# Optimization experiments

Measured on AMD Instinct MI355X. Metric: run time of the kernel, lower is better.

Reference implementation:

```python
import jax, jax.numpy as jnp
import numpy as np

N_NODES = 20000
N_EDGES = 320000
N_GRAPHS = 64
OBS = 64
EDGE_DIM = 16
HEADS = 4
HID = 64
NEG_SLOPE = 0.2
EPS = 1e-16


def _gat_layer(x, src, dst, edge_attr, W, We, att_src, att_dst, att_edge, b):
    """PyG GATConv (concat=True, eval mode: no dropout).
    x: [N, Fin], edge_attr: [E, De], W: [Fin, H*C], We: [De, H*C],
    att_*: [H, C], b: [H*C]. Returns [N, H*C]."""
    N = x.shape[0]
    h = (x @ W).reshape(N, HEADS, HID)                      # [N,H,C]
    he = (edge_attr @ We).reshape(-1, HEADS, HID)           # [E,H,C]
    a_src = jnp.einsum('nhc,hc->nh', h, att_src)            # [N,H]
    a_dst = jnp.einsum('nhc,hc->nh', h, att_dst)
    a_e = jnp.einsum('ehc,hc->eh', he, att_edge)            # [E,H]
    alpha = a_src[src] + a_dst[dst] + a_e                   # [E,H]
    alpha = jax.nn.leaky_relu(alpha, NEG_SLOPE)
    # segment softmax over destination neighborhoods
    m = jax.ops.segment_max(alpha, dst, num_segments=N)     # [N,H]
    m = jnp.where(jnp.isfinite(m), m, 0.0)
    ea = jnp.exp(alpha - m[dst])
    denom = jax.ops.segment_sum(ea, dst, num_segments=N)    # [N,H]
    alpha = ea / (denom[dst] + EPS)
    msg = h[src] * alpha[:, :, None]                        # [E,H,C]
    out = jax.ops.segment_sum(msg, dst, num_segments=N)     # [N,H,C]
    return out.reshape(N, HEADS * HID) + b


def _make_params(key):
    ks = jax.random.split(key, 18)
    p = {}
    dims_in = [OBS, HEADS * HID, HEADS * HID]
    for i in range(3):
        j = i * 6
        fin = dims_in[i]
        p[f'W{i+1}'] = jax.random.normal(ks[j], (fin, HEADS * HID), jnp.float32) * (1.0 / np.sqrt(fin))
        p[f'We{i+1}'] = jax.random.normal(ks[j+1], (EDGE_DIM, HEADS * HID), jnp.float32) * (1.0 / np.sqrt(EDGE_DIM))
        p[f'att_src{i+1}'] = jax.random.normal(ks[j+2], (HEADS, HID), jnp.float32) * 0.1
        p[f'att_dst{i+1}'] = jax.random.normal(ks[j+3], (HEADS, HID), jnp.float32) * 0.1
        p[f'att_edge{i+1}'] = jax.random.normal(ks[j+4], (HEADS, HID), jnp.float32) * 0.1
        p[f'b{i+1}'] = jnp.zeros((HEADS * HID,), jnp.float32)
    return p


def setup_inputs() -> dict:
    key = jax.random.key(0)
    k1, k2, k3, k4, kp = jax.random.split(key, 5)
    inp = {
        'x': jax.random.normal(k1, (N_NODES, OBS), jnp.float32),
        'edge_index': jax.random.randint(k2, (2, N_EDGES), 0, N_NODES, jnp.int64),
        'edge_attr': jax.random.normal(k3, (N_EDGES, EDGE_DIM), jnp.float32),
        'batch': jnp.sort(jax.random.randint(k4, (N_NODES,), 0, N_GRAPHS, jnp.int64)),
    }
    inp.update(_make_params(kp))
    return inp


def reference(x, edge_index, edge_attr, batch,
              W1, We1, att_src1, att_dst1, att_edge1, b1,
              W2, We2, att_src2, att_dst2, att_edge2, b2,
              W3, We3, att_src3, att_dst3, att_edge3, b3):
    src, dst = edge_index[0], edge_index[1]
    h = jax.nn.relu(_gat_layer(x, src, dst, edge_attr, W1, We1, att_src1, att_dst1, att_edge1, b1))
    h = jax.nn.relu(_gat_layer(h, src, dst, edge_attr, W2, We2, att_src2, att_dst2, att_edge2, b2))
    h = jax.nn.relu(_gat_layer(h, src, dst, edge_attr, W3, We3, att_src3, att_dst3, att_edge3, b3))
    # global mean pool over graphs
    sums = jax.ops.segment_sum(h, batch, num_segments=N_GRAPHS)      # [G, H*C]
    counts = jax.ops.segment_sum(jnp.ones((h.shape[0], 1), h.dtype), batch, num_segments=N_GRAPHS)
    pooled = sums / jnp.maximum(counts, 1.0)
    return jnp.tanh(pooled)
```

## Files before the change

kernel.cpp:

```cpp
#include <hip/hip_runtime.h>
#include <hip/hip_bf16.h>
#include <hip/hip_fp16.h>
#include <math.h>

#define N_NODES 20000
#define N_EDGES 320000
#define N_GRAPHS 64
#define OBS 64
#define EDGE_DIM 16
#define HEADS 4
#define HID 64
#define HC 256
#define NEG_SLOPE 0.2f
#define EPSF 1e-16f
#define N_SCAN_BLOCKS ((N_NODES + 255) / 256)
#define CVT_BLOCKS (N_NODES * OBS / 4 / 256)
#define CAP 64

typedef _Float16 f16x8 __attribute__((ext_vector_type(8)));
typedef float f32x4 __attribute__((ext_vector_type(4)));

#define SB_ZERO  N_SCAN_BLOCKS
#define SB_CVT   (SB_ZERO + CVT_BLOCKS)
#define SB_WT0   (SB_CVT + OBS)
#define SB_WT1   (SB_WT0 + HC)
#define SB_WT2   (SB_WT1 + HC)
#define SB_TOT   (SB_WT2 + 3)
__global__ __launch_bounds__(256) void setup_kernel(int* __restrict__ counts,
                                                    float* __restrict__ pooled,
                                                    int* __restrict__ gcounts,
                                                    const float* __restrict__ x, __half* __restrict__ x16,
                                                    const float* __restrict__ W0, const float* __restrict__ W1,
                                                    const float* __restrict__ W2,
                                                    __half* __restrict__ wt0, __half* __restrict__ wt1,
                                                    __half* __restrict__ wt2,
                                                    const float* __restrict__ We0, const float* __restrict__ ae0,
                                                    const float* __restrict__ We1, const float* __restrict__ ae1,
                                                    const float* __restrict__ We2, const float* __restrict__ ae2,
                                                    float* __restrict__ w_eff3) {
    int b = blockIdx.x, t = threadIdx.x;
    if (b < SB_ZERO) {
        int i = b * 256 + t;
        if (i < N_NODES) counts[i] = 0;
        if (i < N_GRAPHS * HC) pooled[i] = 0.f;
        if (i < N_GRAPHS) gcounts[i] = 0;
    } else if (b < SB_CVT) {
        int i = ((b - SB_ZERO) * 256 + t) * 4;
        float4 v = *(const float4*)(x + i);
        *(__half2*)(x16 + i)     = __floats2half2_rn(v.x, v.y);
        *(__half2*)(x16 + i + 2) = __floats2half2_rn(v.z, v.w);
    } else if (b < SB_WT0) {
        int k = b - SB_CVT;
        wt0[(size_t)t * OBS + k] = __float2half(W0[(size_t)k * HC + t]);
    } else if (b < SB_WT1) {
        int k = b - SB_WT0;
        wt1[(size_t)t * HC + k] = __float2half(W1[(size_t)k * HC + t]);
    } else if (b < SB_WT2) {
        int k = b - SB_WT1;
        wt2[(size_t)t * HC + k] = __float2half(W2[(size_t)k * HC + t]);
    } else {
        int l = b - SB_WT2;
        if (t >= 64) return;
        const float* We = (l == 0) ? We0 : (l == 1) ? We1 : We2;
        const float* ae = (l == 0) ? ae0 : (l == 1) ? ae1 : ae2;
        int hh = t >> 4, d = t & 15;
        float acc = 0.f;
        #pragma unroll 8
        for (int c = 0; c < HID; ++c)
            acc += We[d * HC + hh * HID + c] * ae[hh * HID + c];
        w_eff3[l * 64 + hh * 16 + d] = acc;
    }
}

__global__ __launch_bounds__(256) void count_kernel(const int* __restrict__ ei, int* __restrict__ counts) {
    int e = blockIdx.x * 256 + threadIdx.x;
    if (e >= N_EDGES) return;
    atomicAdd(&counts[ei[N_EDGES + e]], 1);
}

__global__ __launch_bounds__(256) void scan_local_kernel(const int* __restrict__ counts,
                                                         int* __restrict__ row_start,
                                                         int* __restrict__ blk_tot) {
    int b = blockIdx.x, t = threadIdx.x;
    int i = b * 256 + t;
    int v = (i < N_NODES) ? counts[i] : 0;
    int lane = t & 63, w = t >> 6;
    int x = v;
    #pragma unroll
    for (int off = 1; off < 64; off <<= 1) {
        int y = __shfl_up(x, off, 64);
        if (lane >= off) x += y;
    }
    __shared__ int wsum[4];
    __shared__ int woff[4];
    if (lane == 63) wsum[w] = x;
    __syncthreads();
    if (t == 0) {
        int s = 0;
        #pragma unroll
        for (int k = 0; k < 4; ++k) { woff[k] = s; s += wsum[k]; }
        blk_tot[b] = s;
    }
    __syncthreads();
    if (i < N_NODES) row_start[i] = x - v + woff[w];
}

__global__ __launch_bounds__(256) void scan_add_kernel(int* __restrict__ row_start,
                                                       const int* __restrict__ blk_tot,
                                                       int* __restrict__ cursor) {
    __shared__ int sd[128];
    int b = blockIdx.x, t = threadIdx.x;
    if (t < 128) sd[t] = (t < b && t < N_SCAN_BLOCKS) ? blk_tot[t] : 0;
    __syncthreads();
    #pragma unroll
    for (int off = 64; off >= 1; off >>= 1) {
        if (t < off) sd[t] += sd[t + off];
        __syncthreads();
    }
    int base = sd[0];
    int i = b * 256 + t;
    if (i < N_NODES) {
        int r = row_start[i] + base;
        row_start[i] = r;
        cursor[i] = r;
    }
}

__global__ __launch_bounds__(256) void fill_ae_kernel(const int* __restrict__ ei,
                                                      const float* __restrict__ edge_attr,
                                                      const float* __restrict__ w_eff3,
                                                      int* __restrict__ cursor,
                                                      int* __restrict__ src_csr,
                                                      float4* __restrict__ ae_csr) {
    __shared__ float wsh[192];
    int t = threadIdx.x;
    if (t < 192) wsh[t] = w_eff3[t];
    __syncthreads();
    int e = blockIdx.x * 256 + t;
    if (e >= N_EDGES) return;
    int s = ei[e];
    int d = ei[N_EDGES + e];
    int pos = atomicAdd(&cursor[d], 1);
    src_csr[pos] = s;
    const float* ea = edge_attr + (size_t)e * EDGE_DIM;
    float x[16];
    #pragma unroll
    for (int i = 0; i < 16; i += 4) {
        float4 v = *(const float4*)(ea + i);
        x[i] = v.x; x[i + 1] = v.y; x[i + 2] = v.z; x[i + 3] = v.w;
    }
    #pragma unroll
    for (int l = 0; l < 3; ++l) {
        float al[4];
        #pragma unroll
        for (int hh = 0; hh < 4; ++hh) {
            float acc = 0.f;
            #pragma unroll
            for (int i = 0; i < 16; ++i) acc += x[i] * wsh[l * 64 + hh * 16 + i];
            al[hh] = acc;
        }
        ae_csr[(size_t)l * N_EDGES + pos] = make_float4(al[0], al[1], al[2], al[3]);
    }
}

template <int NKT>
__global__ __launch_bounds__(256) void gemm16_kernel(const __half* __restrict__ A16,
                                                     const __half* __restrict__ Wt16,
                                                     __half* __restrict__ C16, int M,
                                                     const float* __restrict__ att_src,
                                                     const float* __restrict__ att_dst,
                                                     float* __restrict__ a_src,
                                                     float* __restrict__ a_dst) {
    constexpr int K = NKT * 32;
    __shared__ __align__(16) _Float16 lds[64 * 264];
    int t = threadIdx.x;
    int w = t >> 6, l = t & 63;
    int cg = l & 15, gg = l >> 4;
    int m0 = blockIdx.x * 64;

    {
        int row = (t >> 6) * 16 + (t & 15);
        int k8 = (t >> 4) & 3;
        int rg = m0 + row;
        if (rg >= M) rg = M - 1;
        const _Float16* ag = (const _Float16*)A16 + (size_t)rg * K + k8 * 8;
        f16x8 tmp[NKT];
        #pragma unroll
        for (int j = 0; j < NKT; ++j) tmp[j] = *(const f16x8*)(ag + j * 32);
        #pragma unroll
        for (int j = 0; j < NKT; ++j) *(f16x8*)&lds[(size_t)(j * 256 + t) * 8] = tmp[j];
    }
    __syncthreads();

    f32x4 acc[4][4] = {};
    const _Float16* bg = (const _Float16*)Wt16 + (size_t)(w * 64 + cg) * K + gg * 8;
    #pragma unroll 2
    for (int kt = 0; kt < NKT; ++kt) {
        f16x8 bf[4], af[4];
        #pragma unroll
        for (int ni = 0; ni < 4; ++ni)
            bf[ni] = *(const f16x8*)(bg + (size_t)(ni * 16) * K + kt * 32);
        #pragma unroll
        for (int mi = 0; mi < 4; ++mi)
            af[mi] = *(const f16x8*)&lds[(size_t)(kt * 256 + mi * 64 + l) * 8];
        #pragma unroll
        for (int mi = 0; mi < 4; ++mi)
            #pragma unroll
            for (int ni = 0; ni < 4; ++ni)
                acc[mi][ni] = __builtin_amdgcn_mfma_f32_16x16x32_f16(af[mi], bf[ni], acc[mi][ni], 0, 0, 0);
    }

    {
        float avs[4], avd[4];
        #pragma unroll
        for (int ni = 0; ni < 4; ++ni) {
            avs[ni] = att_src[w * 64 + ni * 16 + cg];
            avd[ni] = att_dst[w * 64 + ni * 16 + cg];
        }
        #pragma unroll
        for (int mi = 0; mi < 4; ++mi)
            #pragma unroll
            for (int reg = 0; reg < 4; ++reg) {
                float ps = acc[mi][0][reg] * avs[0] + acc[mi][1][reg] * avs[1]
                         + acc[mi][2][reg] * avs[2] + acc[mi][3][reg] * avs[3];
                float pd = acc[mi][0][reg] * avd[0] + acc[mi][1][reg] * avd[1]
                         + acc[mi][2][reg] * avd[2] + acc[mi][3][reg] * avd[3];
                #pragma unroll
                for (int o = 1; o < 16; o <<= 1) {
                    ps += __shfl_xor(ps, o, 64);
                    pd += __shfl_xor(pd, o, 64);
                }
                int m = m0 + mi * 16 + gg * 4 + reg;
                if (cg == 0 && m < M) {
                    a_src[(size_t)m * 4 + w] = ps;
                    a_dst[(size_t)m * 4 + w] = pd;
                }
            }
    }

    __syncthreads();
    #pragma unroll
    for (int mi = 0; mi < 4; ++mi)
        #pragma unroll
        for (int ni = 0; ni < 4; ++ni)
            #pragma unroll
            for (int reg = 0; reg < 4; ++reg) {
                int row = mi * 16 + gg * 4 + reg;
                int col = w * 64 + ni * 16 + cg;
                lds[row * 264 + col] = (_Float16)acc[mi][ni][reg];
            }
    __syncthreads();
    #pragma unroll
    for (int i = 0; i < 8; ++i) {
        int g = i * 256 + t;
        int row = g >> 5, cw = g & 31;
        int m = m0 + row;
        if (m < M) {
            f16x8 v = *(const f16x8*)&lds[row * 264 + cw * 8];
            *(f16x8*)((_Float16*)C16 + (size_t)m * HC + cw * 8) = v;
        }
    }
}

__global__ __launch_bounds__(256) void aggregate4_kernel(const int* __restrict__ src_csr,
                                                         const float4* __restrict__ ae_csr,
                                                         const int* __restrict__ row_start,
                                                         const int* __restrict__ counts,
                                                         const float* __restrict__ a_src,
                                                         const float* __restrict__ a_dst,
                                                         const __half* __restrict__ h16,
                                                         const float* __restrict__ bias,
                                                         __half* __restrict__ out16) {
    __shared__ float wlds[4][4][CAP + 1];
    int wid = threadIdx.x >> 6, lane = threadIdx.x & 63;
    int n = blockIdx.x * 4 + wid;
    int start = row_start[n];
    int deg = counts[n];
    const float4* ae = ae_csr + start;
    const int* sp = src_csr + start;
    float4 ad = *(const float4*)(a_dst + (size_t)n * 4);

    float m0 = -INFINITY, m1 = -INFINITY, m2 = -INFINITY, m3 = -INFINITY;
    for (int i = lane; i < deg; i += 64) {
        float4 a = ae[i];
        int s = sp[i];
        float4 as = *(const float4*)(a_src + (size_t)s * 4);
        float v0 = a.x + as.x + ad.x; v0 = v0 > 0.f ? v0 : NEG_SLOPE * v0;
        float v1 = a.y + as.y + ad.y; v1 = v1 > 0.f ? v1 : NEG_SLOPE * v1;
        float v2 = a.z + as.z + ad.z; v2 = v2 > 0.f ? v2 : NEG_SLOPE * v2;
        float v3 = a.w + as.w + ad.w; v3 = v3 > 0.f ? v3 : NEG_SLOPE * v3;
        if (i < CAP) {
            wlds[wid][0][i] = v0; wlds[wid][1][i] = v1;
            wlds[wid][2][i] = v2; wlds[wid][3][i] = v3;
        }
        m0 = fmaxf(m0, v0); m1 = fmaxf(m1, v1);
        m2 = fmaxf(m2, v2); m3 = fmaxf(m3, v3);
    }
    #pragma unroll
    for (int o = 32; o > 0; o >>= 1) {
        m0 = fmaxf(m0, __shfl_xor(m0, o, 64));
        m1 = fmaxf(m1, __shfl_xor(m1, o, 64));
        m2 = fmaxf(m2, __shfl_xor(m2, o, 64));
        m3 = fmaxf(m3, __shfl_xor(m3, o, 64));
    }

    float d0 = 0.f, d1 = 0.f, d2 = 0.f, d3 = 0.f;
    for (int i = lane; i < deg; i += 64) {
        float v0, v1, v2, v3;
        if (i < CAP) {
            v0 = wlds[wid][0][i]; v1 = wlds[wid][1][i];
            v2 = wlds[wid][2][i]; v3 = wlds[wid][3][i];
        } else {
            float4 a = ae[i];
            int s = sp[i];
            float4 as = *(const float4*)(a_src + (size_t)s * 4);
            v0 = a.x + as.x + ad.x; v0 = v0 > 0.f ? v0 : NEG_SLOPE * v0;
            v1 = a.y + as.y + ad.y; v1 = v1 > 0.f ? v1 : NEG_SLOPE * v1;
            v2 = a.z + as.z + ad.z; v2 = v2 > 0.f ? v2 : NEG_SLOPE * v2;
            v3 = a.w + as.w + ad.w; v3 = v3 > 0.f ? v3 : NEG_SLOPE * v3;
        }
        float e0 = __expf(v0 - m0);
        float e1 = __expf(v1 - m1);
        float e2 = __expf(v2 - m2);
        float e3 = __expf(v3 - m3);
        d0 += e0; d1 += e1; d2 += e2; d3 += e3;
        if (i < CAP) {
            wlds[wid][0][i] = e0; wlds[wid][1][i] = e1;
            wlds[wid][2][i] = e2; wlds[wid][3][i] = e3;
        }
    }
    #pragma unroll
    for (int o = 32; o > 0; o >>= 1) {
        d0 += __shfl_xor(d0, o, 64);
        d1 += __shfl_xor(d1, o, 64);
        d2 += __shfl_xor(d2, o, 64);
        d3 += __shfl_xor(d3, o, 64);
    }

    int g = lane >> 5, j = lane & 31;
    int head = j >> 3;
    float mh = (head < 2) ? (head == 0 ? m0 : m1) : (head == 2 ? m2 : m3);
    float dh = (head < 2) ? (head == 0 ? d0 : d1) : (head == 2 ? d2 : d3);
    float adh = (head < 2) ? (head == 0 ? ad.x : ad.y) : (head == 2 ? ad.z : ad.w);

    float acc[8] = {};
    int niter = (deg + 1) >> 1;
    if (deg <= CAP) {
        int it = 0;
        for (; it + 4 <= niter; it += 4) {
            int s_[4]; float w_[4]; f16x8 hv_[4];
            #pragma unroll
            for (int u = 0; u < 4; ++u) {
                int e = (it + u) * 2 + g;
                bool valid = e < deg;
                int ec = valid ? e : deg - 1;
                s_[u] = sp[ec];
                float wv = wlds[wid][head][ec];
                w_[u] = valid ? wv : 0.f;
            }
            #pragma unroll
            for (int u = 0; u < 4; ++u)
                hv_[u] = *(const f16x8*)((const _Float16*)h16 + (size_t)s_[u] * HC + j * 8);
            #pragma unroll
            for (int u = 0; u < 4; ++u)
                #pragma unroll
                for (int q = 0; q < 8; ++q) acc[q] += w_[u] * (float)hv_[u][q];
        }
        for (; it < niter; ++it) {
            int e = it * 2 + g;
            bool valid = e < deg;
            int ec = valid ? e : deg - 1;
            int s = sp[ec];
            float wv = wlds[wid][head][ec];
            float wgt = valid ? wv : 0.f;
            f16x8 hv = *(const f16x8*)((const _Float16*)h16 + (size_t)s * HC + j * 8);
            #pragma unroll
            for (int q = 0; q < 8; ++q) acc[q] += wgt * (float)hv[q];
        }
    } else {
        for (int it = 0; it < niter; ++it) {
            int e = it * 2 + g;
            bool valid = e < deg;
            int ec = valid ? e : deg - 1;
            int s = sp[ec];
            float wgt;
            if (ec < CAP) {
                wgt = wlds[wid][head][ec];
            } else {
                float4 a = ae[ec];
                float aa = (head < 2) ? (head == 0 ? a.x : a.y) : (head == 2 ? a.z : a.w);
                const float* asp = a_src + (size_t)s * 4;
                float v = aa + asp[head] + adh;
                v = v > 0.f ? v : NEG_SLOPE * v;
                wgt = __expf(v - mh);
            }
            if (!valid) wgt = 0.f;
            f16x8 hv = *(const f16x8*)((const _Float16*)h16 + (size_t)s * HC + j * 8);
            #pragma unroll
            for (int q = 0; q < 8; ++q) acc[q] += wgt * (float)hv[q];
        }
    }
    #pragma unroll
    for (int q = 0; q < 8; ++q) acc[q] += __shfl_xor(acc[q], 32, 64);

    if (g == 0) {
        float invd = 1.f / (dh + EPSF);
        float4 b0 = *(const float4*)(bias + j * 8);
        float4 b1 = *(const float4*)(bias + j * 8 + 4);
        float r[8];
        r[0] = fmaxf(acc[0] * invd + b0.x, 0.f);
        r[1] = fmaxf(acc[1] * invd + b0.y, 0.f);
        r[2] = fmaxf(acc[2] * invd + b0.z, 0.f);
        r[3] = fmaxf(acc[3] * invd + b0.w, 0.f);
        r[4] = fmaxf(acc[4] * invd + b1.x, 0.f);
        r[5] = fmaxf(acc[5] * invd + b1.y, 0.f);
        r[6] = fmaxf(acc[6] * invd + b1.z, 0.f);
        r[7] = fmaxf(acc[7] * invd + b1.w, 0.f);
        f16x8 o;
        #pragma unroll
        for (int q = 0; q < 8; ++q) o[q] = (_Float16)r[q];
        *(f16x8*)((_Float16*)out16 + (size_t)n * HC + j * 8) = o;
    }
}

#define NPB 100
__global__ __launch_bounds__(256) void pool_kernel(const __half* __restrict__ h,
                                                   const int* __restrict__ batch,
                                                   float* __restrict__ pooled,
                                                   int* __restrict__ gcounts) {
    int t = threadIdx.x;
    int n0 = blockIdx.x * NPB;
    int n1 = n0 + NPB;
    if (n1 > N_NODES) n1 = N_NODES;
    if (n0 >= N_NODES) return;
    int cur = batch[n0];
    float acc = 0.f;
    int cnt = 0;
    for (int n = n0; n < n1; ++n) {
        int g = batch[n];
        if (g != cur) {
            atomicAdd(&pooled[cur * HC + t], acc);
            if (t == 0) atomicAdd(&gcounts[cur], cnt);
            acc = 0.f; cnt = 0; cur = g;
        }
        acc += __half2float(h[(size_t)n * HC + t]);
        cnt++;
    }
    atomicAdd(&pooled[cur * HC + t], acc);
    if (t == 0) atomicAdd(&gcounts[cur], cnt);
}

__global__ __launch_bounds__(256) void finalize_kernel(const float* __restrict__ pooled,
                                                       const int* __restrict__ gcounts,
                                                       float* __restrict__ out) {
    int g = blockIdx.x, t = threadIdx.x;
    float c = (float)(gcounts[g] > 1 ? gcounts[g] : 1);
    out[g * HC + t] = tanhf(pooled[g * HC + t] / c);
}

extern "C" void kernel_launch(void* const* d_in, const int* in_sizes, int n_in,
                              void* d_out, int out_size, void* d_ws, size_t ws_size,
                              hipStream_t stream) {
    const float* x         = (const float*)d_in[0];
    const int*   ei        = (const int*)d_in[1];
    const float* edge_attr = (const float*)d_in[2];
    const int*   batch     = (const int*)d_in[3];
    const float* Wl[3]  = {(const float*)d_in[4],  (const float*)d_in[10], (const float*)d_in[16]};
    const float* Wel[3] = {(const float*)d_in[5],  (const float*)d_in[11], (const float*)d_in[17]};
    const float* asl[3] = {(const float*)d_in[6],  (const float*)d_in[12], (const float*)d_in[18]};
    const float* adl[3] = {(const float*)d_in[7],  (const float*)d_in[13], (const float*)d_in[19]};
    const float* ael[3] = {(const float*)d_in[8],  (const float*)d_in[14], (const float*)d_in[20]};
    const float* bl[3]  = {(const float*)d_in[9],  (const float*)d_in[15], (const float*)d_in[21]};
    float* out = (float*)d_out;

    char* p = (char*)d_ws;
    auto alloc = [&](size_t bytes) -> void* {
        void* r = (void*)p;
        p += (bytes + 255) & ~(size_t)255;
        return r;
    };
    __half* x16       = (__half*)alloc((size_t)N_NODES * OBS * 2);
    __half* hA16      = (__half*)alloc((size_t)N_NODES * HC * 2);
    __half* hB16      = (__half*)alloc((size_t)N_NODES * HC * 2);
    __half* wt0       = (__half*)alloc((size_t)HC * OBS * 2);
    __half* wt1       = (__half*)alloc((size_t)HC * HC * 2);
    __half* wt2       = (__half*)alloc((size_t)HC * HC * 2);
    float* a_src      = (float*)alloc((size_t)N_NODES * 4 * 4);
    float* a_dst      = (float*)alloc((size_t)N_NODES * 4 * 4);
    float4* ae_csr    = (float4*)alloc((size_t)3 * N_EDGES * 16);
    int* counts       = (int*)alloc((size_t)N_NODES * 4);
    int* row_start    = (int*)alloc((size_t)N_NODES * 4);
    int* cursor       = (int*)alloc((size_t)N_NODES * 4);
    int* src_csr      = (int*)alloc((size_t)N_EDGES * 4);
    float* w_eff3     = (float*)alloc(192 * 4);
    float* pooled     = (float*)alloc((size_t)N_GRAPHS * HC * 4);
    int* gcounts      = (int*)alloc((size_t)N_GRAPHS * 4);
    int* blk_tot      = (int*)alloc((size_t)N_SCAN_BLOCKS * 4);

    setup_kernel<<<SB_TOT, 256, 0, stream>>>(counts, pooled, gcounts, x, x16,
                                             Wl[0], Wl[1], Wl[2], wt0, wt1, wt2,
                                             Wel[0], ael[0], Wel[1], ael[1], Wel[2], ael[2],
                                             w_eff3);

    count_kernel<<<N_EDGES / 256, 256, 0, stream>>>(ei, counts);
    scan_local_kernel<<<N_SCAN_BLOCKS, 256, 0, stream>>>(counts, row_start, blk_tot);
    scan_add_kernel<<<N_SCAN_BLOCKS, 256, 0, stream>>>(row_start, blk_tot, cursor);
    fill_ae_kernel<<<N_EDGES / 256, 256, 0, stream>>>(ei, edge_attr, w_eff3, cursor,
                                                      src_csr, ae_csr);

    const int ngrid = (N_NODES + 63) / 64;
    const __half* wtl[3] = {wt0, wt1, wt2};
    const __half* cur_in = x16;
    for (int l = 0; l < 3; ++l) {
        if (l == 0)
            gemm16_kernel<2><<<ngrid, 256, 0, stream>>>(cur_in, wtl[l], hA16, N_NODES,
                                                        asl[l], adl[l], a_src, a_dst);
        else
            gemm16_kernel<8><<<ngrid, 256, 0, stream>>>(cur_in, wtl[l], hA16, N_NODES,
                                                        asl[l], adl[l], a_src, a_dst);
        aggregate4_kernel<<<N_NODES / 4, 256, 0, stream>>>(src_csr, ae_csr + (size_t)l * N_EDGES,
                                                           row_start, counts, a_src, a_dst,
                                                           hA16, bl[l], hB16);
        cur_in = hB16;
    }

    pool_kernel<<<(N_NODES + NPB - 1) / NPB, 256, 0, stream>>>(hB16, batch, pooled, gcounts);
    finalize_kernel<<<N_GRAPHS, 256, 0, stream>>>(pooled, gcounts, out);
}
```

Measured before the change: 226.5 us.

## Reorder layer-1 GAT as aggregate-then-transform using linearity of projection

For the first layer, attention logits are computed directly from the 64-wide input via precomputed W·att vectors. The per-head softmax-weighted aggregation then runs over 64-dim fp16 input rows instead of 256-dim projected rows, producing a per-head aggregated tensor. A block-diagonal MFMA GEMM applies W per head and fuses bias plus ReLU. This cuts the bytes gathered per edge in layer 1, at the cost of an extra small kernel and a different rounding order.

```diff
diff --git a/kernel.cpp b/kernel.cpp
--- a/kernel.cpp
+++ b/kernel.cpp
@@ -25,7 +25,8 @@
 #define SB_WT0   (SB_CVT + OBS)
 #define SB_WT1   (SB_WT0 + HC)
 #define SB_WT2   (SB_WT1 + HC)
-#define SB_TOT   (SB_WT2 + 3)
+#define SB_WEFF  (SB_WT2 + 3)
+#define SB_TOT   (SB_WEFF + 2)
 __global__ __launch_bounds__(256) void setup_kernel(int* __restrict__ counts,
                                                     float* __restrict__ pooled,
                                                     int* __restrict__ gcounts,
@@ -37,7 +38,9 @@
                                                     const float* __restrict__ We0, const float* __restrict__ ae0,
                                                     const float* __restrict__ We1, const float* __restrict__ ae1,
                                                     const float* __restrict__ We2, const float* __restrict__ ae2,
-                                                    float* __restrict__ w_eff3) {
+                                                    float* __restrict__ w_eff3,
+                                                    const float* __restrict__ as0, const float* __restrict__ ad0,
+                                                    float* __restrict__ wsd0) {
     int b = blockIdx.x, t = threadIdx.x;
     if (b < SB_ZERO) {
         int i = b * 256 + t;
@@ -58,7 +61,7 @@
     } else if (b < SB_WT2) {
         int k = b - SB_WT1;
         wt2[(size_t)t * HC + k] = __float2half(W2[(size_t)k * HC + t]);
-    } else {
+    } else if (b < SB_WEFF) {
         int l = b - SB_WT2;
         if (t >= 64) return;
         const float* We = (l == 0) ? We0 : (l == 1) ? We1 : We2;
@@ -69,6 +72,16 @@
         for (int c = 0; c < HID; ++c)
             acc += We[d * HC + hh * HID + c] * ae[hh * HID + c];
         w_eff3[l * 64 + hh * 16 + d] = acc;
+    } else {
+        int idx = (b - SB_WEFF) * 256 + t;
+        int k = idx >> 3, jj = idx & 7;
+        int h = jj & 3;
+        const float* att = (jj < 4) ? as0 : ad0;
+        float acc = 0.f;
+        #pragma unroll 8
+        for (int c = 0; c < HID; ++c)
+            acc += W0[(size_t)k * HC + h * HID + c] * att[h * HID + c];
+        wsd0[k * 8 + jj] = acc;
     }
 }
 
@@ -160,6 +173,283 @@
             al[hh] = acc;
         }
         ae_csr[(size_t)l * N_EDGES + pos] = make_float4(al[0], al[1], al[2], al[3]);
+    }
+}
+
+__global__ __launch_bounds__(256) void asd0_kernel(const __half* __restrict__ x16,
+                                                   const float* __restrict__ wsd0,
+                                                   float* __restrict__ a_src,
+                                                   float* __restrict__ a_dst) {
+    __shared__ float wsd[512];
+    int t = threadIdx.x;
+    wsd[t] = wsd0[t];
+    wsd[t + 256] = wsd0[t + 256];
+    __syncthreads();
+    int wv = t >> 6, lane = t & 63;
+    int g = lane >> 3, j = lane & 7;
+    int n = blockIdx.x * 32 + wv * 8 + g;
+    f16x8 xv = *(const f16x8*)((const _Float16*)x16 + (size_t)n * OBS + j * 8);
+    float s[8] = {};
+    #pragma unroll
+    for (int q = 0; q < 8; ++q) {
+        float xq = (float)xv[q];
+        #pragma unroll
+        for (int jj = 0; jj < 8; ++jj) s[jj] += xq * wsd[(j * 8 + q) * 8 + jj];
+    }
+    #pragma unroll
+    for (int o = 1; o < 8; o <<= 1)
+        #pragma unroll
+        for (int jj = 0; jj < 8; ++jj) s[jj] += __shfl_xor(s[jj], o, 64);
+    if (j == 0) {
+        *(float4*)(a_src + (size_t)n * 4) = make_float4(s[0], s[1], s[2], s[3]);
+        *(float4*)(a_dst + (size_t)n * 4) = make_float4(s[4], s[5], s[6], s[7]);
+    }
+}
+
+__global__ __launch_bounds__(256) void agg64_kernel(const int* __restrict__ src_csr,
+                                                    const float4* __restrict__ ae_csr,
+                                                    const int* __restrict__ row_start,
+                                                    const int* __restrict__ counts,
+                                                    const float* __restrict__ a_src,
+                                                    const float* __restrict__ a_dst,
+                                                    const __half* __restrict__ x16,
+                                                    __half* __restrict__ xt16) {
+    __shared__ float wlds[4][4][CAP + 1];
+    int wid = threadIdx.x >> 6, lane = threadIdx.x & 63;
+    int n = blockIdx.x * 4 + wid;
+    int start = row_start[n];
+    int deg = counts[n];
+    const float4* ae = ae_csr + start;
+    const int* sp = src_csr + start;
+    float4 ad = *(const float4*)(a_dst + (size_t)n * 4);
+
+    float m0 = -INFINITY, m1 = -INFINITY, m2 = -INFINITY, m3 = -INFINITY;
+    for (int i = lane; i < deg; i += 64) {
+        float4 a = ae[i];
+        int s = sp[i];
+        float4 as = *(const float4*)(a_src + (size_t)s * 4);
+        float v0 = a.x + as.x + ad.x; v0 = v0 > 0.f ? v0 : NEG_SLOPE * v0;
+        float v1 = a.y + as.y + ad.y; v1 = v1 > 0.f ? v1 : NEG_SLOPE * v1;
+        float v2 = a.z + as.z + ad.z; v2 = v2 > 0.f ? v2 : NEG_SLOPE * v2;
+        float v3 = a.w + as.w + ad.w; v3 = v3 > 0.f ? v3 : NEG_SLOPE * v3;
+        if (i < CAP) {
+            wlds[wid][0][i] = v0; wlds[wid][1][i] = v1;
+            wlds[wid][2][i] = v2; wlds[wid][3][i] = v3;
+        }
+        m0 = fmaxf(m0, v0); m1 = fmaxf(m1, v1);
+        m2 = fmaxf(m2, v2); m3 = fmaxf(m3, v3);
+    }
+    #pragma unroll
+    for (int o = 32; o > 0; o >>= 1) {
+        m0 = fmaxf(m0, __shfl_xor(m0, o, 64));
+        m1 = fmaxf(m1, __shfl_xor(m1, o, 64));
+        m2 = fmaxf(m2, __shfl_xor(m2, o, 64));
+        m3 = fmaxf(m3, __shfl_xor(m3, o, 64));
+    }
+
+    float d0 = 0.f, d1 = 0.f, d2 = 0.f, d3 = 0.f;
+    for (int i = lane; i < deg; i += 64) {
+        float v0, v1, v2, v3;
+        if (i < CAP) {
+            v0 = wlds[wid][0][i]; v1 = wlds[wid][1][i];
+            v2 = wlds[wid][2][i]; v3 = wlds[wid][3][i];
+        } else {
+            float4 a = ae[i];
+            int s = sp[i];
+            float4 as = *(const float4*)(a_src + (size_t)s * 4);
+            v0 = a.x + as.x + ad.x; v0 = v0 > 0.f ? v0 : NEG_SLOPE * v0;
+            v1 = a.y + as.y + ad.y; v1 = v1 > 0.f ? v1 : NEG_SLOPE * v1;
+            v2 = a.z + as.z + ad.z; v2 = v2 > 0.f ? v2 : NEG_SLOPE * v2;
+            v3 = a.w + as.w + ad.w; v3 = v3 > 0.f ? v3 : NEG_SLOPE * v3;
+        }
+        float e0 = __expf(v0 - m0);
+        float e1 = __expf(v1 - m1);
+        float e2 = __expf(v2 - m2);
+        float e3 = __expf(v3 - m3);
+        d0 += e0; d1 += e1; d2 += e2; d3 += e3;
+        if (i < CAP) {
+            wlds[wid][0][i] = e0; wlds[wid][1][i] = e1;
+            wlds[wid][2][i] = e2; wlds[wid][3][i] = e3;
+        }
+    }
+    #pragma unroll
+    for (int o = 32; o > 0; o >>= 1) {
+        d0 += __shfl_xor(d0, o, 64);
+        d1 += __shfl_xor(d1, o, 64);
+        d2 += __shfl_xor(d2, o, 64);
+        d3 += __shfl_xor(d3, o, 64);
+    }
+
+    int g = lane >> 3, j = lane & 7;
+    float ac0[8] = {}, ac1[8] = {}, ac2[8] = {}, ac3[8] = {};
+    int niter = (deg + 7) >> 3;
+    if (deg <= CAP) {
+        int it = 0;
+        for (; it + 2 <= niter; it += 2) {
+            int s_[2]; float w0_[2], w1_[2], w2_[2], w3_[2]; f16x8 hv_[2];
+            #pragma unroll
+            for (int u = 0; u < 2; ++u) {
+                int e = (it + u) * 8 + g;
+                bool valid = e < deg;
+                int ec = valid ? e : deg - 1;
+                s_[u] = sp[ec];
+                float z = valid ? 1.f : 0.f;
+                w0_[u] = wlds[wid][0][ec] * z; w1_[u] = wlds[wid][1][ec] * z;
+                w2_[u] = wlds[wid][2][ec] * z; w3_[u] = wlds[wid][3][ec] * z;
+            }
+            #pragma unroll
+            for (int u = 0; u < 2; ++u)
+                hv_[u] = *(const f16x8*)((const _Float16*)x16 + (size_t)s_[u] * OBS + j * 8);
+            #pragma unroll
+            for (int u = 0; u < 2; ++u)
+                #pragma unroll
+                for (int q = 0; q < 8; ++q) {
+                    float xv = (float)hv_[u][q];
+                    ac0[q] += w0_[u] * xv; ac1[q] += w1_[u] * xv;
+                    ac2[q] += w2_[u] * xv; ac3[q] += w3_[u] * xv;
+                }
+        }
+        for (; it < niter; ++it) {
+            int e = it * 8 + g;
+            bool valid = e < deg;
+            int ec = valid ? e : deg - 1;
+            int s = sp[ec];
+            float z = valid ? 1.f : 0.f;
+            float w0 = wlds[wid][0][ec] * z, w1 = wlds[wid][1][ec] * z;
+            float w2 = wlds[wid][2][ec] * z, w3 = wlds[wid][3][ec] * z;
+            f16x8 hv = *(const f16x8*)((const _Float16*)x16 + (size_t)s * OBS + j * 8);
+            #pragma unroll
+            for (int q = 0; q < 8; ++q) {
+                float xv = (float)hv[q];
+                ac0[q] += w0 * xv; ac1[q] += w1 * xv;
+                ac2[q] += w2 * xv; ac3[q] += w3 * xv;
+            }
+        }
+    } else {
+        for (int it = 0; it < niter; ++it) {
+            int e = it * 8 + g;
+            bool valid = e < deg;
+            int ec = valid ? e : deg - 1;
+            int s = sp[ec];
+            float w0, w1, w2, w3;
+            if (ec < CAP) {
+                w0 = wlds[wid][0][ec]; w1 = wlds[wid][1][ec];
+                w2 = wlds[wid][2][ec]; w3 = wlds[wid][3][ec];
+            } else {
+                float4 a = ae[ec];
+                float4 as = *(const float4*)(a_src + (size_t)s * 4);
+                float v0 = a.x + as.x + ad.x; v0 = v0 > 0.f ? v0 : NEG_SLOPE * v0;
+                float v1 = a.y + as.y + ad.y; v1 = v1 > 0.f ? v1 : NEG_SLOPE * v1;
+                float v2 = a.z + as.z + ad.z; v2 = v2 > 0.f ? v2 : NEG_SLOPE * v2;
+                float v3 = a.w + as.w + ad.w; v3 = v3 > 0.f ? v3 : NEG_SLOPE * v3;
+                w0 = __expf(v0 - m0); w1 = __expf(v1 - m1);
+                w2 = __expf(v2 - m2); w3 = __expf(v3 - m3);
+            }
+            if (!valid) { w0 = w1 = w2 = w3 = 0.f; }
+            f16x8 hv = *(const f16x8*)((const _Float16*)x16 + (size_t)s * OBS + j * 8);
+            #pragma unroll
+            for (int q = 0; q < 8; ++q) {
+                float xv = (float)hv[q];
+                ac0[q] += w0 * xv; ac1[q] += w1 * xv;
+                ac2[q] += w2 * xv; ac3[q] += w3 * xv;
+            }
+        }
+    }
+    #pragma unroll
+    for (int o = 8; o < 64; o <<= 1)
+        #pragma unroll
+        for (int q = 0; q < 8; ++q) {
+            ac0[q] += __shfl_xor(ac0[q], o, 64);
+            ac1[q] += __shfl_xor(ac1[q], o, 64);
+            ac2[q] += __shfl_xor(ac2[q], o, 64);
+            ac3[q] += __shfl_xor(ac3[q], o, 64);
+        }
+    if (g == 0) {
+        float i0 = 1.f / (d0 + EPSF), i1 = 1.f / (d1 + EPSF);
+        float i2 = 1.f / (d2 + EPSF), i3 = 1.f / (d3 + EPSF);
+        _Float16* o = (_Float16*)xt16 + (size_t)n * HC;
+        f16x8 r0, r1, r2, r3;
+        #pragma unroll
+        for (int q = 0; q < 8; ++q) {
+            r0[q] = (_Float16)(ac0[q] * i0);
+            r1[q] = (_Float16)(ac1[q] * i1);
+            r2[q] = (_Float16)(ac2[q] * i2);
+            r3[q] = (_Float16)(ac3[q] * i3);
+        }
+        *(f16x8*)(o + j * 8)        = r0;
+        *(f16x8*)(o + 64 + j * 8)   = r1;
+        *(f16x8*)(o + 128 + j * 8)  = r2;
+        *(f16x8*)(o + 192 + j * 8)  = r3;
+    }
+}
+
+__global__ __launch_bounds__(256) void gemm0bd_kernel(const __half* __restrict__ XT,
+                                                      const __half* __restrict__ Wt0,
+                                                      const float* __restrict__ bias,
+                                                      __half* __restrict__ Z16, int M) {
+    __shared__ __align__(16) _Float16 lds[64 * 264];
+    int t = threadIdx.x;
+    int w = t >> 6, l = t & 63;
+    int cg = l & 15, gg = l >> 4;
+    int m0 = blockIdx.x * 64;
+
+    {
+        int row = (t >> 6) * 16 + (t & 15);
+        int k8 = (t >> 4) & 3;
+        int rg = m0 + row;
+        if (rg >= M) rg = M - 1;
+        const _Float16* ag = (const _Float16*)XT + (size_t)rg * HC + k8 * 8;
+        f16x8 tmp[8];
+        #pragma unroll
+        for (int j = 0; j < 8; ++j) tmp[j] = *(const f16x8*)(ag + j * 32);
+        #pragma unroll
+        for (int j = 0; j < 8; ++j) *(f16x8*)&lds[(size_t)(j * 256 + t) * 8] = tmp[j];
+    }
+    __syncthreads();
+
+    f32x4 acc[4][4] = {};
+    const _Float16* bg = (const _Float16*)Wt0 + (size_t)(w * 64 + cg) * OBS + gg * 8;
+    #pragma unroll
+    for (int ktp = 0; ktp < 2; ++ktp) {
+        int kt = w * 2 + ktp;
+        f16x8 bf[4], af[4];
+        #pragma unroll
+        for (int ni = 0; ni < 4; ++ni)
+            bf[ni] = *(const f16x8*)(bg + (size_t)(ni * 16) * OBS + ktp * 32);
+        #pragma unroll
+        for (int mi = 0; mi < 4; ++mi)
+            af[mi] = *(const f16x8*)&lds[(size_t)(kt * 256 + mi * 64 + l) * 8];
+        #pragma unroll
+        for (int mi = 0; mi < 4; ++mi)
+            #pragma unroll
+            for (int ni = 0; ni < 4; ++ni)
+                acc[mi][ni] = __builtin_amdgcn_mfma_f32_16x16x32_f16(af[mi], bf[ni], acc[mi][ni], 0, 0, 0);
+    }
+
+    float bv[4];
+    #pragma unroll
+    for (int ni = 0; ni < 4; ++ni) bv[ni] = bias[w * 64 + ni * 16 + cg];
+    __syncthreads();
+    #pragma unroll
+    for (int mi = 0; mi < 4; ++mi)
+        #pragma unroll
+        for (int ni = 0; ni < 4; ++ni)
+            #pragma unroll
+            for (int reg = 0; reg < 4; ++reg) {
+                int row = mi * 16 + gg * 4 + reg;
+                int col = w * 64 + ni * 16 + cg;
+                lds[row * 264 + col] = (_Float16)fmaxf(acc[mi][ni][reg] + bv[ni], 0.f);
+            }
+    __syncthreads();
+    #pragma unroll
+    for (int i = 0; i < 8; ++i) {
+        int gi = i * 256 + t;
+        int row = gi >> 5, cw = gi & 31;
+        int m = m0 + row;
+        if (m < M) {
+            f16x8 v = *(const f16x8*)&lds[row * 264 + cw * 8];
+            *(f16x8*)((_Float16*)Z16 + (size_t)m * HC + cw * 8) = v;
+        }
     }
 }
 
@@ -493,6 +783,7 @@
     int* cursor       = (int*)alloc((size_t)N_NODES * 4);
     int* src_csr      = (int*)alloc((size_t)N_EDGES * 4);
     float* w_eff3     = (float*)alloc(192 * 4);
+    float* wsd0       = (float*)alloc(512 * 4);
     float* pooled     = (float*)alloc((size_t)N_GRAPHS * HC * 4);
     int* gcounts      = (int*)alloc((size_t)N_GRAPHS * 4);
     int* blk_tot      = (int*)alloc((size_t)N_SCAN_BLOCKS * 4);
@@ -500,7 +791,7 @@
     setup_kernel<<<SB_TOT, 256, 0, stream>>>(counts, pooled, gcounts, x, x16,
                                              Wl[0], Wl[1], Wl[2], wt0, wt1, wt2,
                                              Wel[0], ael[0], Wel[1], ael[1], Wel[2], ael[2],
-                                             w_eff3);
+                                             w_eff3, asl[0], adl[0], wsd0);
 
     count_kernel<<<N_EDGES / 256, 256, 0, stream>>>(ei, counts);
     scan_local_kernel<<<N_SCAN_BLOCKS, 256, 0, stream>>>(counts, row_start, blk_tot);
@@ -509,19 +800,19 @@
                                                       src_csr, ae_csr);
 
     const int ngrid = (N_NODES + 63) / 64;
-    const __half* wtl[3] = {wt0, wt1, wt2};
-    const __half* cur_in = x16;
-    for (int l = 0; l < 3; ++l) {
-        if (l == 0)
-            gemm16_kernel<2><<<ngrid, 256, 0, stream>>>(cur_in, wtl[l], hA16, N_NODES,
-                                                        asl[l], adl[l], a_src, a_dst);
-        else
-            gemm16_kernel<8><<<ngrid, 256, 0, stream>>>(cur_in, wtl[l], hA16, N_NODES,
-                                                        asl[l], adl[l], a_src, a_dst);
+
+    asd0_kernel<<<N_NODES / 32, 256, 0, stream>>>(x16, wsd0, a_src, a_dst);
+    agg64_kernel<<<N_NODES / 4, 256, 0, stream>>>(src_csr, ae_csr, row_start, counts,
+                                                  a_src, a_dst, x16, hA16);
+    gemm0bd_kernel<<<ngrid, 256, 0, stream>>>(hA16, wt0, bl[0], hB16, N_NODES);
+
+    for (int l = 1; l < 3; ++l) {
+        const __half* wtl = (l == 1) ? wt1 : wt2;
+        gemm16_kernel<8><<<ngrid, 256, 0, stream>>>(hB16, wtl, hA16, N_NODES,
+                                                    asl[l], adl[l], a_src, a_dst);
         aggregate4_kernel<<<N_NODES / 4, 256, 0, stream>>>(src_csr, ae_csr + (size_t)l * N_EDGES,
                                                            row_start, counts, a_src, a_dst,
                                                            hA16, bl[l], hB16);
-        cur_in = hB16;
     }
 
     pool_kernel<<<(N_NODES + NPB - 1) / NPB, 256, 0, stream>>>(hB16, batch, pooled, gcounts);
```

After: 234.8 us. 1.04x slower.
